# Kernel optimization log

Hardware: AMD Instinct MI355X
Metric: run time of the kernel (lower is better)

The kernel has to match this reference:

```python
import jax, jax.numpy as jnp
import numpy as np

N_SPEAKERS, N_UTTER, EMB_DIM = 1024, 20, 256


def setup_inputs() -> dict:
    key = jax.random.key(0)
    k_in, = jax.random.split(key, 1)
    inp = jax.random.normal(k_in, (N_SPEAKERS, N_UTTER, EMB_DIM), dtype=jnp.float32)
    w = jnp.asarray(10.0, dtype=jnp.float32)
    b = jnp.asarray(-5.0, dtype=jnp.float32)
    return {"input": inp, "w": w, "b": b}


def reference(input, w, b):
    # input: [N, M, D] utterance embeddings
    N, M, D = input.shape
    centroids = jnp.mean(input, axis=1)                       # [N, D]
    # leave-one-out centroid for each (speaker, utterance):
    # mean of the other M-1 utterances of the same speaker
    excl = (centroids[:, None, :] * M - input) / (M - 1)      # [N, M, D]

    inv_u = 1.0 / jnp.linalg.norm(input, axis=-1, keepdims=True)      # [N, M, 1]
    u_hat = input * inv_u                                             # [N, M, D]
    c_hat = centroids / jnp.linalg.norm(centroids, axis=-1, keepdims=True)  # [N, D]
    e_hat = excl / jnp.linalg.norm(excl, axis=-1, keepdims=True)      # [N, M, D]

    # cosine sim of every utterance vs every full centroid
    cs = jnp.einsum('nmd,kd->nmk', u_hat, c_hat)              # [N, M, N]
    # override k == own speaker with the excluded-centroid cosine
    cs_self = jnp.sum(u_hat * e_hat, axis=-1)                 # [N, M]
    idx = jnp.arange(N)
    cs = cs.at[idx, :, idx].set(cs_self)

    sim = w * cs + b                                          # scaled similarity
    logp = jax.nn.log_softmax(sim, axis=-1)                   # softmax over speakers
    loss = -jnp.sum(logp[idx, :, idx])
    return loss
```

## Files before the change

### kernel.cpp

```cpp
#include <hip/hip_runtime.h>


#define D_DIM 256
#define N_SPK 1024
#define M_UTT 20

typedef __bf16 bf16x8 __attribute__((ext_vector_type(8)));
typedef float f32x16 __attribute__((ext_vector_type(16)));

__device__ __forceinline__ float block_sum256(float v, float* red, int tid) {
#pragma unroll
  for (int o = 32; o; o >>= 1) v += __shfl_xor(v, o, 64);
  __syncthreads();
  if ((tid & 63) == 0) red[tid >> 6] = v;
  __syncthreads();
  return red[0] + red[1] + red[2] + red[3];
}

__global__ __launch_bounds__(256) void ge2e_prep(
    const float* __restrict__ inp, __bf16* __restrict__ bsw,
    float* __restrict__ c_raw, float* __restrict__ ccv,
    float* __restrict__ out) {
  const int n = blockIdx.x, d = threadIdx.x;
  if (n == 0 && d == 0) out[0] = 0.0f;
  __shared__ float red[4];

  const float* up = inp + (size_t)n * (M_UTT * D_DIM) + d;
  float s = 0.0f;
#pragma unroll
  for (int m = 0; m < M_UTT; ++m) s += up[(size_t)m * D_DIM];
  const float c = s * (1.0f / (float)M_UTT);
  c_raw[(size_t)n * D_DIM + d] = c;

  const float cc = block_sum256(c * c, red, d);
  if (d == 0) ccv[n] = cc;

  const int tile = n >> 5, n5 = n & 31, ks = d >> 4, half = (d >> 3) & 1,
            j = d & 7;
  bsw[(size_t)(((tile * 16 + ks) * 64 + half * 32 + n5) * 8 + j)] =
      (__bf16)(c * rsqrtf(cc));
}

__global__ __launch_bounds__(256, 2) void ge2e_main(
    const float* __restrict__ inp, const float* __restrict__ wp,
    const __bf16* __restrict__ bsw, const float* __restrict__ c_raw,
    const float* __restrict__ ccv, float* __restrict__ out) {
  __shared__ __align__(16) __bf16 lA[32 * D_DIM];
  __shared__ float uuL[32], ucL[32], ccL[32], a2L[32];
  __shared__ float rowtot[4][32];
  const int tid = threadIdx.x;
  const int r0 = blockIdx.x * 32;
  const float w = wp[0];

  {
    const int m = tid >> 3, seg = tid & 7;
    const int r = r0 + m, nr = r / M_UTT;
    const float* urow = inp + (size_t)r * D_DIM + seg * 32;
    const float* crow = c_raw + (size_t)nr * D_DIM + seg * 32;
    float uu = 0.f, uc = 0.f;
    bf16x8* lAv = reinterpret_cast<bf16x8*>(lA);
#pragma unroll
    for (int t = 0; t < 4; ++t) {
      const float4 f0 = reinterpret_cast<const float4*>(urow)[2 * t];
      const float4 f1 = reinterpret_cast<const float4*>(urow)[2 * t + 1];
      const float4 c0 = reinterpret_cast<const float4*>(crow)[2 * t];
      const float4 c1 = reinterpret_cast<const float4*>(crow)[2 * t + 1];
      uu += f0.x * f0.x + f0.y * f0.y + f0.z * f0.z + f0.w * f0.w +
            f1.x * f1.x + f1.y * f1.y + f1.z * f1.z + f1.w * f1.w;
      uc += f0.x * c0.x + f0.y * c0.y + f0.z * c0.z + f0.w * c0.w +
            f1.x * c1.x + f1.y * c1.y + f1.z * c1.z + f1.w * c1.w;
      bf16x8 pk;
      pk[0] = (__bf16)f0.x; pk[1] = (__bf16)f0.y;
      pk[2] = (__bf16)f0.z; pk[3] = (__bf16)f0.w;
      pk[4] = (__bf16)f1.x; pk[5] = (__bf16)f1.y;
      pk[6] = (__bf16)f1.z; pk[7] = (__bf16)f1.w;
      const int k = seg * 32 + t * 8;
      lAv[(k >> 4) * 64 + ((k >> 3) & 1) * 32 + m] = pk;
    }
#pragma unroll
    for (int o = 1; o < 8; o <<= 1) {
      uu += __shfl_xor(uu, o, 64);
      uc += __shfl_xor(uc, o, 64);
    }
    if (seg == 0) {
      uuL[m] = uu;
      ucL[m] = uc;
      ccL[m] = ccv[nr];
      a2L[m] = w * rsqrtf(uu);
    }
  }
  __syncthreads();

  const int lane = tid & 63, wv = tid >> 6, hl = lane >> 5;
  const bf16x8* lAv = reinterpret_cast<const bf16x8*>(lA);
  bf16x8 A[16];
#pragma unroll
  for (int ks = 0; ks < 16; ++ks) A[ks] = lAv[ks * 64 + lane];

  float a2v[16];
#pragma unroll
  for (int i = 0; i < 16; ++i)
    a2v[i] = a2L[(i & 3) + 8 * (i >> 2) + 4 * hl];

  float sume[16];
#pragma unroll
  for (int i = 0; i < 16; ++i) sume[i] = 0.0f;

  const bf16x8* Bv = reinterpret_cast<const bf16x8*>(bsw);
  for (int t = 0; t < 8; ++t) {
    const int tg = wv * 8 + t;
    const bf16x8* Bt = Bv + (size_t)tg * 1024 + lane;
    f32x16 acc0, acc1;
#pragma unroll
    for (int i = 0; i < 16; ++i) { acc0[i] = 0.0f; acc1[i] = 0.0f; }
#pragma unroll
    for (int ks = 0; ks < 8; ++ks) {
      acc0 = __builtin_amdgcn_mfma_f32_32x32x16_bf16(A[2 * ks], Bt[(2 * ks) * 64],
                                                     acc0, 0, 0, 0);
      acc1 = __builtin_amdgcn_mfma_f32_32x32x16_bf16(A[2 * ks + 1],
                                                     Bt[(2 * ks + 1) * 64],
                                                     acc1, 0, 0, 0);
    }
#pragma unroll
    for (int i = 0; i < 16; ++i)
      sume[i] += __expf(a2v[i] * (acc0[i] + acc1[i]));
  }

#pragma unroll
  for (int i = 0; i < 16; ++i) {
    float v = sume[i];
#pragma unroll
    for (int o = 1; o < 32; o <<= 1) v += __shfl_xor(v, o, 64);
    sume[i] = v;
  }
  if ((lane & 31) == 0) {
#pragma unroll
    for (int i = 0; i < 16; ++i)
      rowtot[wv][(i & 3) + 8 * (i >> 2) + 4 * hl] = sume[i];
  }
  __syncthreads();

  if (tid < 32) {
    const float se0 = rowtot[0][tid] + rowtot[1][tid] + rowtot[2][tid] +
                      rowtot[3][tid];
    const float uu = uuL[tid], uc = ucL[tid], cc = ccL[tid];
    const float Mf = (float)M_UTT;
    const float ue = (Mf * uc - uu) * (1.0f / (Mf - 1.0f));
    const float ee = (Mf * Mf * cc - 2.0f * Mf * uc + uu) *
                     (1.0f / ((Mf - 1.0f) * (Mf - 1.0f)));
    const float sself = w * ue * rsqrtf(uu * ee);
    const float sown = w * uc * rsqrtf(uu * cc);
    const float se = se0 + __expf(sself) - __expf(sown);
    float v = __logf(se) - sself;
#pragma unroll
    for (int o = 1; o < 32; o <<= 1) v += __shfl_xor(v, o, 64);
    if (tid == 0) atomicAdd(out, v);
  }
}

extern "C" void kernel_launch(void* const* d_in, const int* in_sizes, int n_in,
                              void* d_out, int out_size, void* d_ws, size_t ws_size,
                              hipStream_t stream) {
  const float* inp = (const float*)d_in[0];
  const float* wp  = (const float*)d_in[1];
  float* out = (float*)d_out;

  __bf16* bsw  = (__bf16*)d_ws;
  float* c_raw = (float*)((char*)d_ws + 512 * 1024);
  float* ccv   = c_raw + (size_t)N_SPK * D_DIM;

  ge2e_prep<<<N_SPK, 256, 0, stream>>>(inp, bsw, c_raw, ccv, out);
  ge2e_main<<<(N_SPK * M_UTT) / 32, 256, 0, stream>>>(inp, wp, bsw, c_raw, ccv,
                                                      out);
}
```

Before: 98.18 us.

## Switch similarity GEMM to FP8 MFMA with pre-scaled operands and B prefetch

Normalized centroids and scaled utterance rows (w/||u||) are now quantized to FP8 e4m3 and multiplied with the fp8 32x32x16 MFMA, which halves operand bytes and raises matrix throughput compared with bf16. The prep kernel is restructured to one wavefront per speaker with float4 loads and a wave-only reduction. The main loop double-buffers B tile loads across iterations, and the per-row scale is folded into A, removing the multiply before exp. FP8 quantization of the scaled A values (magnitude up to about w) costs accuracy in the logits, and clamps were added to guard exp and log.

```diff
diff --git a/kernel.cpp b/kernel.cpp
--- a/kernel.cpp
+++ b/kernel.cpp
@@ -1,52 +1,69 @@
 #include <hip/hip_runtime.h>
+#include <hip/hip_fp8.h>
 
 
 #define D_DIM 256
 #define N_SPK 1024
 #define M_UTT 20
 
-typedef __bf16 bf16x8 __attribute__((ext_vector_type(8)));
+typedef long lx2 __attribute__((ext_vector_type(2)));
 typedef float f32x16 __attribute__((ext_vector_type(16)));
 
-__device__ __forceinline__ float block_sum256(float v, float* red, int tid) {
-#pragma unroll
-  for (int o = 32; o; o >>= 1) v += __shfl_xor(v, o, 64);
-  __syncthreads();
-  if ((tid & 63) == 0) red[tid >> 6] = v;
-  __syncthreads();
-  return red[0] + red[1] + red[2] + red[3];
+__device__ __forceinline__ int pk4_fp8(float x0, float x1, float x2, float x3) {
+#if __has_builtin(__builtin_amdgcn_cvt_pk_fp8_f32)
+  int v = __builtin_amdgcn_cvt_pk_fp8_f32(x0, x1, 0, false);
+  v = __builtin_amdgcn_cvt_pk_fp8_f32(x2, x3, v, true);
+  return v;
+#else
+  union { int i; unsigned char b[4]; } u;
+  u.b[0] = __hip_fp8_e4m3(x0).__x;
+  u.b[1] = __hip_fp8_e4m3(x1).__x;
+  u.b[2] = __hip_fp8_e4m3(x2).__x;
+  u.b[3] = __hip_fp8_e4m3(x3).__x;
+  return u.i;
+#endif
 }
 
 __global__ __launch_bounds__(256) void ge2e_prep(
-    const float* __restrict__ inp, __bf16* __restrict__ bsw,
+    const float* __restrict__ inp, unsigned int* __restrict__ bsw32,
     float* __restrict__ c_raw, float* __restrict__ ccv,
     float* __restrict__ out) {
-  const int n = blockIdx.x, d = threadIdx.x;
-  if (n == 0 && d == 0) out[0] = 0.0f;
-  __shared__ float red[4];
-
-  const float* up = inp + (size_t)n * (M_UTT * D_DIM) + d;
-  float s = 0.0f;
-#pragma unroll
-  for (int m = 0; m < M_UTT; ++m) s += up[(size_t)m * D_DIM];
-  const float c = s * (1.0f / (float)M_UTT);
-  c_raw[(size_t)n * D_DIM + d] = c;
-
-  const float cc = block_sum256(c * c, red, d);
-  if (d == 0) ccv[n] = cc;
-
-  const int tile = n >> 5, n5 = n & 31, ks = d >> 4, half = (d >> 3) & 1,
-            j = d & 7;
-  bsw[(size_t)(((tile * 16 + ks) * 64 + half * 32 + n5) * 8 + j)] =
-      (__bf16)(c * rsqrtf(cc));
+  const int tid = threadIdx.x, lane = tid & 63, wv = tid >> 6;
+  const int s = blockIdx.x * 4 + wv;
+  if (blockIdx.x == 0 && tid == 0) out[0] = 0.0f;
+
+  const float4* up =
+      reinterpret_cast<const float4*>(inp + (size_t)s * (M_UTT * D_DIM)) + lane;
+  float4 a = make_float4(0.f, 0.f, 0.f, 0.f);
+#pragma unroll
+  for (int m = 0; m < M_UTT; ++m) {
+    const float4 f = up[m * (D_DIM / 4)];
+    a.x += f.x; a.y += f.y; a.z += f.z; a.w += f.w;
+  }
+  const float inv = 1.0f / (float)M_UTT;
+  const float4 c = make_float4(a.x * inv, a.y * inv, a.z * inv, a.w * inv);
+  reinterpret_cast<float4*>(c_raw + (size_t)s * D_DIM)[lane] = c;
+
+  float cc = c.x * c.x + c.y * c.y + c.z * c.z + c.w * c.w;
+#pragma unroll
+  for (int o = 1; o < 64; o <<= 1) cc += __shfl_xor(cc, o, 64);
+  if (lane == 0) ccv[s] = cc;
+
+  const float r = rsqrtf(fmaxf(cc, 1e-20f));
+  const int q = pk4_fp8(c.x * r, c.y * r, c.z * r, c.w * r);
+  const int t = s >> 5, n5 = s & 31;
+  const int p = lane >> 3, sub = (lane >> 2) & 1;
+  const int half = (lane >> 1) & 1, jb = (lane & 1) * 4;
+  bsw32[((((t * 8 + p) * 64) + half * 32 + n5) * 16 + sub * 8 + jb) >> 2] =
+      (unsigned int)q;
 }
 
 __global__ __launch_bounds__(256, 2) void ge2e_main(
     const float* __restrict__ inp, const float* __restrict__ wp,
-    const __bf16* __restrict__ bsw, const float* __restrict__ c_raw,
+    const unsigned char* __restrict__ bsw, const float* __restrict__ c_raw,
     const float* __restrict__ ccv, float* __restrict__ out) {
-  __shared__ __align__(16) __bf16 lA[32 * D_DIM];
-  __shared__ float uuL[32], ucL[32], ccL[32], a2L[32];
+  __shared__ __align__(16) unsigned char lA[32 * D_DIM];
+  __shared__ float uuL[32], ucL[32], ccL[32];
   __shared__ float rowtot[4][32];
   const int tid = threadIdx.x;
   const int r0 = blockIdx.x * 32;
@@ -55,75 +72,85 @@
   {
     const int m = tid >> 3, seg = tid & 7;
     const int r = r0 + m, nr = r / M_UTT;
-    const float* urow = inp + (size_t)r * D_DIM + seg * 32;
-    const float* crow = c_raw + (size_t)nr * D_DIM + seg * 32;
+    const float4* urow =
+        reinterpret_cast<const float4*>(inp + (size_t)r * D_DIM + seg * 32);
+    const float4* crow =
+        reinterpret_cast<const float4*>(c_raw + (size_t)nr * D_DIM + seg * 32);
+    float4 uf[8];
     float uu = 0.f, uc = 0.f;
-    bf16x8* lAv = reinterpret_cast<bf16x8*>(lA);
-#pragma unroll
-    for (int t = 0; t < 4; ++t) {
-      const float4 f0 = reinterpret_cast<const float4*>(urow)[2 * t];
-      const float4 f1 = reinterpret_cast<const float4*>(urow)[2 * t + 1];
-      const float4 c0 = reinterpret_cast<const float4*>(crow)[2 * t];
-      const float4 c1 = reinterpret_cast<const float4*>(crow)[2 * t + 1];
-      uu += f0.x * f0.x + f0.y * f0.y + f0.z * f0.z + f0.w * f0.w +
-            f1.x * f1.x + f1.y * f1.y + f1.z * f1.z + f1.w * f1.w;
-      uc += f0.x * c0.x + f0.y * c0.y + f0.z * c0.z + f0.w * c0.w +
-            f1.x * c1.x + f1.y * c1.y + f1.z * c1.z + f1.w * c1.w;
-      bf16x8 pk;
-      pk[0] = (__bf16)f0.x; pk[1] = (__bf16)f0.y;
-      pk[2] = (__bf16)f0.z; pk[3] = (__bf16)f0.w;
-      pk[4] = (__bf16)f1.x; pk[5] = (__bf16)f1.y;
-      pk[6] = (__bf16)f1.z; pk[7] = (__bf16)f1.w;
-      const int k = seg * 32 + t * 8;
-      lAv[(k >> 4) * 64 + ((k >> 3) & 1) * 32 + m] = pk;
+#pragma unroll
+    for (int q = 0; q < 8; ++q) {
+      uf[q] = urow[q];
+      const float4 cf = crow[q];
+      uu += uf[q].x * uf[q].x + uf[q].y * uf[q].y + uf[q].z * uf[q].z +
+            uf[q].w * uf[q].w;
+      uc += uf[q].x * cf.x + uf[q].y * cf.y + uf[q].z * cf.z + uf[q].w * cf.w;
     }
 #pragma unroll
     for (int o = 1; o < 8; o <<= 1) {
       uu += __shfl_xor(uu, o, 64);
       uc += __shfl_xor(uc, o, 64);
     }
+    const float s = w * rsqrtf(fmaxf(uu, 1e-20f));
+    int4 ch0, ch1;
+    ch0.x = pk4_fp8(s * uf[0].x, s * uf[0].y, s * uf[0].z, s * uf[0].w);
+    ch0.y = pk4_fp8(s * uf[1].x, s * uf[1].y, s * uf[1].z, s * uf[1].w);
+    ch0.z = pk4_fp8(s * uf[4].x, s * uf[4].y, s * uf[4].z, s * uf[4].w);
+    ch0.w = pk4_fp8(s * uf[5].x, s * uf[5].y, s * uf[5].z, s * uf[5].w);
+    ch1.x = pk4_fp8(s * uf[2].x, s * uf[2].y, s * uf[2].z, s * uf[2].w);
+    ch1.y = pk4_fp8(s * uf[3].x, s * uf[3].y, s * uf[3].z, s * uf[3].w);
+    ch1.z = pk4_fp8(s * uf[6].x, s * uf[6].y, s * uf[6].z, s * uf[6].w);
+    ch1.w = pk4_fp8(s * uf[7].x, s * uf[7].y, s * uf[7].z, s * uf[7].w);
+    reinterpret_cast<int4*>(lA)[seg * 64 + m] = ch0;
+    reinterpret_cast<int4*>(lA)[seg * 64 + m + 32] = ch1;
     if (seg == 0) {
       uuL[m] = uu;
       ucL[m] = uc;
       ccL[m] = ccv[nr];
-      a2L[m] = w * rsqrtf(uu);
     }
   }
   __syncthreads();
 
   const int lane = tid & 63, wv = tid >> 6, hl = lane >> 5;
-  const bf16x8* lAv = reinterpret_cast<const bf16x8*>(lA);
-  bf16x8 A[16];
-#pragma unroll
-  for (int ks = 0; ks < 16; ++ks) A[ks] = lAv[ks * 64 + lane];
-
-  float a2v[16];
-#pragma unroll
-  for (int i = 0; i < 16; ++i)
-    a2v[i] = a2L[(i & 3) + 8 * (i >> 2) + 4 * hl];
+  lx2 A[8];
+  const lx2* lAv = reinterpret_cast<const lx2*>(lA);
+#pragma unroll
+  for (int p = 0; p < 8; ++p) A[p] = lAv[p * 64 + lane];
 
   float sume[16];
 #pragma unroll
   for (int i = 0; i < 16; ++i) sume[i] = 0.0f;
 
-  const bf16x8* Bv = reinterpret_cast<const bf16x8*>(bsw);
+  const lx2* Bbase =
+      reinterpret_cast<const lx2*>(bsw) + (size_t)(wv * 8) * 512 + lane;
+  lx2 Bc[8];
+#pragma unroll
+  for (int p = 0; p < 8; ++p) Bc[p] = Bbase[p * 64];
+#pragma unroll
   for (int t = 0; t < 8; ++t) {
-    const int tg = wv * 8 + t;
-    const bf16x8* Bt = Bv + (size_t)tg * 1024 + lane;
+    lx2 Bn[8];
+    if (t < 7) {
+      const lx2* Bt = Bbase + (t + 1) * 512;
+#pragma unroll
+      for (int p = 0; p < 8; ++p) Bn[p] = Bt[p * 64];
+    }
     f32x16 acc0, acc1;
 #pragma unroll
     for (int i = 0; i < 16; ++i) { acc0[i] = 0.0f; acc1[i] = 0.0f; }
 #pragma unroll
-    for (int ks = 0; ks < 8; ++ks) {
-      acc0 = __builtin_amdgcn_mfma_f32_32x32x16_bf16(A[2 * ks], Bt[(2 * ks) * 64],
-                                                     acc0, 0, 0, 0);
-      acc1 = __builtin_amdgcn_mfma_f32_32x32x16_bf16(A[2 * ks + 1],
-                                                     Bt[(2 * ks + 1) * 64],
-                                                     acc1, 0, 0, 0);
+    for (int p = 0; p < 8; ++p) {
+      acc0 = __builtin_amdgcn_mfma_f32_32x32x16_fp8_fp8(A[p].x, Bc[p].x, acc0,
+                                                        0, 0, 0);
+      acc1 = __builtin_amdgcn_mfma_f32_32x32x16_fp8_fp8(A[p].y, Bc[p].y, acc1,
+                                                        0, 0, 0);
     }
 #pragma unroll
     for (int i = 0; i < 16; ++i)
-      sume[i] += __expf(a2v[i] * (acc0[i] + acc1[i]));
+      sume[i] += __expf(fminf(acc0[i] + acc1[i], 40.0f));
+    if (t < 7) {
+#pragma unroll
+      for (int p = 0; p < 8; ++p) Bc[p] = Bn[p];
+    }
   }
 
 #pragma unroll
@@ -148,9 +175,10 @@
     const float ue = (Mf * uc - uu) * (1.0f / (Mf - 1.0f));
     const float ee = (Mf * Mf * cc - 2.0f * Mf * uc + uu) *
                      (1.0f / ((Mf - 1.0f) * (Mf - 1.0f)));
-    const float sself = w * ue * rsqrtf(uu * ee);
-    const float sown = w * uc * rsqrtf(uu * cc);
-    const float se = se0 + __expf(sself) - __expf(sown);
+    const float sself = w * ue * rsqrtf(fmaxf(uu * ee, 1e-20f));
+    const float sown = w * uc * rsqrtf(fmaxf(uu * cc, 1e-20f));
+    const float se = fmaxf(
+        se0 + __expf(fminf(sself, 40.f)) - __expf(fminf(sown, 40.f)), 1e-10f);
     float v = __logf(se) - sself;
 #pragma unroll
     for (int o = 1; o < 32; o <<= 1) v += __shfl_xor(v, o, 64);
@@ -165,11 +193,12 @@
   const float* wp  = (const float*)d_in[1];
   float* out = (float*)d_out;
 
-  __bf16* bsw  = (__bf16*)d_ws;
-  float* c_raw = (float*)((char*)d_ws + 512 * 1024);
+  unsigned char* bsw = (unsigned char*)d_ws;
+  float* c_raw = (float*)((char*)d_ws + 256 * 1024);
   float* ccv   = c_raw + (size_t)N_SPK * D_DIM;
 
-  ge2e_prep<<<N_SPK, 256, 0, stream>>>(inp, bsw, c_raw, ccv, out);
+  ge2e_prep<<<N_SPK / 4, 256, 0, stream>>>(inp, (unsigned int*)bsw, c_raw, ccv,
+                                           out);
   ge2e_main<<<(N_SPK * M_UTT) / 32, 256, 0, stream>>>(inp, wp, bsw, c_raw, ccv,
                                                       out);
 }
```

Result: faster. 92.34 us (-5.9%).
